# Kernel tuning notes

Hardware: AMD Instinct MI355X
Metric: run time of the kernel (lower is better)

## Reference

```python
import jax, jax.numpy as jnp
import numpy as np

B, D, K, P = 512, 2048, 128, 5

def setup_inputs() -> dict:
    key = jax.random.key(0)
    k1, k2 = jax.random.split(key)
    x = jax.random.normal(k1, (B, D), dtype=jnp.float32)
    theta = 0.05 * jax.random.normal(k2, (D, K, P), dtype=jnp.float32)
    log_weight_scale = jnp.zeros((K, P), dtype=jnp.float32)
    bias = -jnp.ones((K,), dtype=jnp.float32)  # layer inits bias to -1
    return {"x": x, "theta": theta, "log_weight_scale": log_weight_scale, "bias": bias}

def reference(x, theta, log_weight_scale, bias):
    b = x.shape[0]
    # weight-normalized kernel: [D, K, P]
    norm = jnp.sqrt(jnp.sum(theta * theta, axis=0))            # [K, P]
    kernel = theta * (jnp.exp(log_weight_scale) / norm)[None]  # [D, K, P]
    actv = jnp.einsum('bd,dkp->bkp', x, kernel)                # [B, K, P]
    # pairwise L1 over P: [B, K, B]
    diff = jnp.abs(actv[:, :, :, None] - jnp.transpose(actv, (1, 2, 0))[None])  # [B,K,P,B]
    abs_dif = jnp.sum(diff, axis=2) + 1e6 * jnp.eye(b, dtype=x.dtype)[:, None, :]
    f = jnp.sum(jnp.exp(-abs_dif), axis=2) + bias[None, :]     # [B, K]
    return jnp.concatenate([x, f], axis=1)                     # [B, D+K]
```

## Files before the change

### kernel.cpp

```cpp
#include <hip/hip_runtime.h>
#include <math.h>

#define BSZ 512
#define DD 2048
#define KK 128
#define PP 5
#define NCOL (KK * PP)
#define OUTW (DD + KK)
#define LOG2E 1.4426950408889634f

#define KSPLIT 16
#define GM 64
#define GN 64
#define GK (DD / KSPLIT)
#define GBK 32
#define QSPLIT 8

#define WS_NORM 0
#define WS_ACTV (WS_NORM + NCOL)
#define WS_FPART (WS_ACTV + BSZ * NCOL)
#define WS_PART (WS_FPART + QSPLIT * KK * BSZ)

__global__ __launch_bounds__(256) void norm_kernel(const float* __restrict__ theta,
                                                   float* __restrict__ norm) {
    int i   = blockIdx.x * 256 + threadIdx.x;
    int col = i % NCOL;
    int seg = i / NCOL;
    const float* p = theta + (size_t)seg * 16 * NCOL + col;
    float s = 0.f;
#pragma unroll
    for (int j = 0; j < 16; ++j) {
        float v = p[(size_t)j * NCOL];
        s += v * v;
    }
    atomicAdd(&norm[col], s);
}

__global__ __launch_bounds__(256) void gemm_kernel(const float* __restrict__ x,
                                                   const float* __restrict__ theta,
                                                   float* __restrict__ part) {
    __shared__ float xT[GBK][GM];

    const int t    = threadIdx.x;
    const int lane = t & 63;
    const int wave = t >> 6;
    const int m    = blockIdx.y * GM + lane;
    const int kz   = blockIdx.z * GK;
    const int nw = __builtin_amdgcn_readfirstlane(blockIdx.x * GN + wave * 16);

    const float* xrow = x + (size_t)m * DD;

    float acc[16] = {};

    float4 v0 = *(const float4*)&xrow[kz + wave * 8];
    float4 v1 = *(const float4*)&xrow[kz + wave * 8 + 4];

    for (int kc = kz; kc < kz + GK; kc += GBK) {
        __syncthreads();
        xT[wave * 8 + 0][lane] = v0.x;
        xT[wave * 8 + 1][lane] = v0.y;
        xT[wave * 8 + 2][lane] = v0.z;
        xT[wave * 8 + 3][lane] = v0.w;
        xT[wave * 8 + 4][lane] = v1.x;
        xT[wave * 8 + 5][lane] = v1.y;
        xT[wave * 8 + 6][lane] = v1.z;
        xT[wave * 8 + 7][lane] = v1.w;
        __syncthreads();

        if (kc + GBK < kz + GK) {
            v0 = *(const float4*)&xrow[kc + GBK + wave * 8];
            v1 = *(const float4*)&xrow[kc + GBK + wave * 8 + 4];
        }

        const float* th = &theta[(size_t)kc * NCOL + nw];
#pragma unroll 4
        for (int kk = 0; kk < GBK; ++kk) {
            const float a = xT[kk][lane];
#pragma unroll
            for (int j = 0; j < 16; ++j)
                acc[j] += a * th[(size_t)kk * NCOL + j];
        }
    }

    float* dst = part + (size_t)blockIdx.z * (BSZ * NCOL) + (size_t)m * NCOL + nw;
    *(float4*)&dst[0]  = make_float4(acc[0],  acc[1],  acc[2],  acc[3]);
    *(float4*)&dst[4]  = make_float4(acc[4],  acc[5],  acc[6],  acc[7]);
    *(float4*)&dst[8]  = make_float4(acc[8],  acc[9],  acc[10], acc[11]);
    *(float4*)&dst[12] = make_float4(acc[12], acc[13], acc[14], acc[15]);
}

__global__ __launch_bounds__(256) void reduce_kernel(const float* __restrict__ part,
                                                     const float* __restrict__ norm,
                                                     const float* __restrict__ lws,
                                                     float* __restrict__ actv) {
    int i   = blockIdx.x * 256 + threadIdx.x;
    int col = i % NCOL;
    float s = 0.f;
#pragma unroll
    for (int q = 0; q < KSPLIT; ++q)
        s += part[(size_t)q * (BSZ * NCOL) + i];
    const float scale = __builtin_amdgcn_exp2f(lws[col] * LOG2E) *
                        __builtin_amdgcn_rsqf(norm[col]) * LOG2E;
    actv[i] = s * scale;
}

__global__ __launch_bounds__(128) void pairwise_kernel(const float* __restrict__ actv,
                                                       float* __restrict__ f_part) {
    const int k   = blockIdx.x;
    const int q   = blockIdx.y;
    const int tid = threadIdx.x;

    __shared__ float sB[64][8];

    for (int i = tid; i < 64 * PP; i += 128) {
        int r = i / PP;
        int p = i - r * PP;
        sB[r][p] = actv[(size_t)(q * 64 + r) * NCOL + k * PP + p];
    }

    float a[4][PP];
#pragma unroll
    for (int r = 0; r < 4; ++r) {
        const float* ap = &actv[(size_t)(tid + r * 128) * NCOL + k * PP];
#pragma unroll
        for (int p = 0; p < PP; ++p) a[r][p] = ap[p];
    }
    __syncthreads();

    float acc[4] = {0.f, 0.f, 0.f, 0.f};
#pragma unroll 2
    for (int j = 0; j < 64; ++j) {
        const float4 v  = *(const float4*)&sB[j][0];
        const float  v4 = sB[j][4];
#pragma unroll
        for (int r = 0; r < 4; ++r) {
            float s = fabsf(a[r][0] - v.x) + fabsf(a[r][1] - v.y) +
                      fabsf(a[r][2] - v.z) + fabsf(a[r][3] - v.w) +
                      fabsf(a[r][4] - v4);
            acc[r] += __builtin_amdgcn_exp2f(-s);
        }
    }

    float* fp = f_part + ((size_t)q * KK + k) * BSZ;
#pragma unroll
    for (int r = 0; r < 4; ++r)
        fp[tid + r * 128] = acc[r];
}

__global__ __launch_bounds__(256) void epilogue_kernel(const float* __restrict__ x,
                                                       const float* __restrict__ f_part,
                                                       const float* __restrict__ bias,
                                                       float* __restrict__ out) {
    const int bid = blockIdx.x;
    if (bid < 1024) {
        int i = bid * 256 + threadIdx.x;
        int r = i >> 9;
        int c = i & 511;
        float4 v = *(const float4*)&x[(size_t)r * DD + c * 4];
        *(float4*)&out[(size_t)r * OUTW + c * 4] = v;
    } else {
        int i = (bid - 1024) * 256 + threadIdx.x;
        int k = i >> 9;
        int b = i & 511;
        float s = 0.f;
#pragma unroll
        for (int q = 0; q < QSPLIT; ++q)
            s += f_part[((size_t)q * KK + k) * BSZ + b];
        out[(size_t)b * OUTW + DD + k] = s - 1.0f + bias[k];
    }
}

extern "C" void kernel_launch(void* const* d_in, const int* in_sizes, int n_in,
                              void* d_out, int out_size, void* d_ws, size_t ws_size,
                              hipStream_t stream) {
    const float* x     = (const float*)d_in[0];
    const float* theta = (const float*)d_in[1];
    const float* lws   = (const float*)d_in[2];
    const float* bias  = (const float*)d_in[3];
    float* out = (float*)d_out;

    float* ws     = (float*)d_ws;
    float* norm   = ws + WS_NORM;
    float* actv   = ws + WS_ACTV;
    float* f_part = ws + WS_FPART;
    float* part   = ws + WS_PART;

    hipMemsetAsync(norm, 0, NCOL * sizeof(float), stream);

    norm_kernel<<<320, 256, 0, stream>>>(theta, norm);
    gemm_kernel<<<dim3(NCOL / GN, BSZ / GM, KSPLIT), 256, 0, stream>>>(x, theta, part);
    reduce_kernel<<<(BSZ * NCOL) / 256, 256, 0, stream>>>(part, norm, lws, actv);
    pairwise_kernel<<<dim3(KK, QSPLIT), 128, 0, stream>>>(actv, f_part);
    epilogue_kernel<<<1280, 256, 0, stream>>>(x, f_part, bias, out);
}
```

Baseline: 123.4 us.

## Fold epilogue into earlier kernels, drop memset, atomically accumulate pairwise sums

```diff
diff --git a/kernel.cpp b/kernel.cpp
--- a/kernel.cpp
+++ b/kernel.cpp
@@ -18,28 +18,48 @@
 
 #define WS_NORM 0
 #define WS_ACTV (WS_NORM + NCOL)
-#define WS_FPART (WS_ACTV + BSZ * NCOL)
-#define WS_PART (WS_FPART + QSPLIT * KK * BSZ)
+#define WS_PART (WS_ACTV + BSZ * NCOL)
 
 __global__ __launch_bounds__(256) void norm_kernel(const float* __restrict__ theta,
                                                    float* __restrict__ norm) {
-    int i   = blockIdx.x * 256 + threadIdx.x;
-    int col = i % NCOL;
-    int seg = i / NCOL;
-    const float* p = theta + (size_t)seg * 16 * NCOL + col;
+    __shared__ float partial[32][8];
+    const int t   = threadIdx.x;
+    const int c8  = blockIdx.x * 8;
+    const int col = c8 + (t & 7);
+    const int g   = t >> 3;
+    const float* p = theta + (size_t)g * NCOL + col;
     float s = 0.f;
 #pragma unroll
-    for (int j = 0; j < 16; ++j) {
-        float v = p[(size_t)j * NCOL];
+    for (int j = 0; j < 64; ++j) {
+        float v = p[(size_t)j * 32 * NCOL];
         s += v * v;
     }
-    atomicAdd(&norm[col], s);
+    partial[g][t & 7] = s;
+    __syncthreads();
+    if (t < 8) {
+        float acc = 0.f;
+#pragma unroll
+        for (int gg = 0; gg < 32; ++gg) acc += partial[gg][t];
+        norm[c8 + t] = acc;
+    }
 }
 
 __global__ __launch_bounds__(256) void gemm_kernel(const float* __restrict__ x,
                                                    const float* __restrict__ theta,
-                                                   float* __restrict__ part) {
+                                                   float* __restrict__ part,
+                                                   float* __restrict__ out) {
     __shared__ float xT[GBK][GM];
+
+    if (blockIdx.z == KSPLIT) {
+        const int bid = blockIdx.y * (NCOL / GN) + blockIdx.x;
+        for (int i = bid * 256 + threadIdx.x; i < BSZ * (DD / 4); i += 80 * 256) {
+            int r = i >> 9;
+            int c = i & 511;
+            float4 v = *(const float4*)&x[(size_t)r * DD + c * 4];
+            *(float4*)&out[(size_t)r * OUTW + c * 4] = v;
+        }
+        return;
+    }
 
     const int t    = threadIdx.x;
     const int lane = t & 63;
@@ -92,7 +112,16 @@
 __global__ __launch_bounds__(256) void reduce_kernel(const float* __restrict__ part,
                                                      const float* __restrict__ norm,
                                                      const float* __restrict__ lws,
-                                                     float* __restrict__ actv) {
+                                                     const float* __restrict__ bias,
+                                                     float* __restrict__ actv,
+                                                     float* __restrict__ out) {
+    if (blockIdx.x >= (BSZ * NCOL) / 256) {
+        int i = (blockIdx.x - (BSZ * NCOL) / 256) * 256 + threadIdx.x;
+        int b = i >> 7;
+        int k = i & 127;
+        out[(size_t)b * OUTW + DD + k] = bias[k] - 1.0f;
+        return;
+    }
     int i   = blockIdx.x * 256 + threadIdx.x;
     int col = i % NCOL;
     float s = 0.f;
@@ -105,7 +134,7 @@
 }
 
 __global__ __launch_bounds__(128) void pairwise_kernel(const float* __restrict__ actv,
-                                                       float* __restrict__ f_part) {
+                                                       float* __restrict__ out) {
     const int k   = blockIdx.x;
     const int q   = blockIdx.y;
     const int tid = threadIdx.x;
@@ -141,33 +170,9 @@
         }
     }
 
-    float* fp = f_part + ((size_t)q * KK + k) * BSZ;
 #pragma unroll
     for (int r = 0; r < 4; ++r)
-        fp[tid + r * 128] = acc[r];
-}
-
-__global__ __launch_bounds__(256) void epilogue_kernel(const float* __restrict__ x,
-                                                       const float* __restrict__ f_part,
-                                                       const float* __restrict__ bias,
-                                                       float* __restrict__ out) {
-    const int bid = blockIdx.x;
-    if (bid < 1024) {
-        int i = bid * 256 + threadIdx.x;
-        int r = i >> 9;
-        int c = i & 511;
-        float4 v = *(const float4*)&x[(size_t)r * DD + c * 4];
-        *(float4*)&out[(size_t)r * OUTW + c * 4] = v;
-    } else {
-        int i = (bid - 1024) * 256 + threadIdx.x;
-        int k = i >> 9;
-        int b = i & 511;
-        float s = 0.f;
-#pragma unroll
-        for (int q = 0; q < QSPLIT; ++q)
-            s += f_part[((size_t)q * KK + k) * BSZ + b];
-        out[(size_t)b * OUTW + DD + k] = s - 1.0f + bias[k];
-    }
+        atomicAdd(&out[(size_t)(tid + r * 128) * OUTW + DD + k], acc[r]);
 }
 
 extern "C" void kernel_launch(void* const* d_in, const int* in_sizes, int n_in,
@@ -179,17 +184,13 @@
     const float* bias  = (const float*)d_in[3];
     float* out = (float*)d_out;
 
-    float* ws     = (float*)d_ws;
-    float* norm   = ws + WS_NORM;
-    float* actv   = ws + WS_ACTV;
-    float* f_part = ws + WS_FPART;
-    float* part   = ws + WS_PART;
+    float* ws   = (float*)d_ws;
+    float* norm = ws + WS_NORM;
+    float* actv = ws + WS_ACTV;
+    float* part = ws + WS_PART;
 
-    hipMemsetAsync(norm, 0, NCOL * sizeof(float), stream);
-
-    norm_kernel<<<320, 256, 0, stream>>>(theta, norm);
-    gemm_kernel<<<dim3(NCOL / GN, BSZ / GM, KSPLIT), 256, 0, stream>>>(x, theta, part);
-    reduce_kernel<<<(BSZ * NCOL) / 256, 256, 0, stream>>>(part, norm, lws, actv);
-    pairwise_kernel<<<dim3(KK, QSPLIT), 128, 0, stream>>>(actv, f_part);
-    epilogue_kernel<<<1280, 256, 0, stream>>>(x, f_part, bias, out);
+    norm_kernel<<<80, 256, 0, stream>>>(theta, norm);
+    gemm_kernel<<<dim3(NCOL / GN, BSZ / GM, KSPLIT + 1), 256, 0, stream>>>(x, theta, part, out);
+    reduce_kernel<<<(BSZ * NCOL) / 256 + 256, 256, 0, stream>>>(part, norm, lws, bias, actv, out);
+    pairwise_kernel<<<dim3(KK, QSPLIT), 128, 0, stream>>>(actv, out);
 }
```

Result: slower. 153.5 us (+24.5%).
